# Kernel optimization log

Measured on AMD Instinct MI355X. Metric: run time of the kernel, lower is better.

The kernel has to match this reference:

```python
import jax, jax.numpy as jnp
import numpy as np

B, LT, D, H, DI = 8, 128, 512, 8, 2048
NMEM, LMEM = 1024, 64
DH = D // H
EPS = 1e-5
NEG = -1e9

def _ln(x, g, b):
    mu = x.mean(-1, keepdims=True)
    var = ((x - mu) ** 2).mean(-1, keepdims=True)
    return (x - mu) * jax.lax.rsqrt(var + EPS) * g + b

def _ffn(x, W1, b1, W2, b2):
    # PositionwiseFF with residual=True (dropout=0 / eval)
    return x + jax.nn.relu(x @ W1 + b1) @ W2 + b2

def setup_inputs():
    key = jax.random.key(0)
    ks = jax.random.split(key, 16)
    w = lambda i, shape: jax.random.normal(ks[i], shape, jnp.float32) * 0.02
    return {
        "dec_output": jax.random.normal(ks[0], (B, LT, D), jnp.float32),
        "mem_attn_out": jax.random.normal(ks[1], (B, LT, NMEM + 1), jnp.float32),
        "enc_out_mem": jax.random.normal(ks[2], (NMEM, LMEM, D), jnp.float32),
        "tgt_emb_mem": jax.random.normal(ks[3], (NMEM, LMEM, D), jnp.float32),
        "tgt_mask_mem": jax.random.randint(ks[4], (NMEM, LMEM), 0, 2, jnp.int32),
        "tgt_mask": jax.random.randint(ks[5], (B, LT), 0, 2, jnp.int32),
        "g0": jnp.ones((D,), jnp.float32), "be0": jnp.zeros((D,), jnp.float32),
        "g1": jnp.ones((D,), jnp.float32), "be1": jnp.zeros((D,), jnp.float32),
        "Wq": w(6, (D, D)), "bq": jnp.zeros((D,), jnp.float32),
        "Wk": w(7, (D, D)), "bk": jnp.zeros((D,), jnp.float32),
        "Wv": w(8, (D, D)), "bv": jnp.zeros((D,), jnp.float32),
        "Wo": w(9, (D, D)), "bo": jnp.zeros((D,), jnp.float32),
        "f1W1": w(10, (D, DI)), "f1b1": jnp.zeros((DI,), jnp.float32),
        "f1W2": w(11, (DI, D)), "f1b2": jnp.zeros((D,), jnp.float32),
        "f2W1": w(12, (D, DI)), "f2b1": jnp.zeros((DI,), jnp.float32),
        "f2W2": w(13, (DI, D)), "f2b2": jnp.zeros((D,), jnp.float32),
    }

def reference(dec_output, mem_attn_out, enc_out_mem, tgt_emb_mem, tgt_mask_mem, tgt_mask,
              g0, be0, g1, be1, Wq, bq, Wk, bk, Wv, bv, Wo, bo,
              f1W1, f1b1, f1W2, f1b2, f2W1, f2b1, f2W2, f2b2):
    x = _ln(dec_output, g0, be0)                       # [B,LT,D]
    N = B * LT
    samples = jnp.argmax(mem_attn_out, -1).reshape(N) - 1   # [-1, NMEM-1]
    valid = samples >= 0                               # [N]
    s = jnp.maximum(samples, 0)                        # clamp; masked later
    q = x.reshape(N, 1, D)
    # gather memory per selected query (torch compacts via unique; same math)
    k_in = enc_out_mem[s]                              # [N,LMEM,D]
    v_in = tgt_emb_mem[s]                              # [N,LMEM,D]
    kmask = tgt_mask_mem[s] != 0                       # True = valid key
    # multi-head attention, residual=True
    qh = (q @ Wq + bq).reshape(N, 1, H, DH).transpose(0, 2, 1, 3)     # [N,H,1,DH]
    kh = (k_in @ Wk + bk).reshape(N, LMEM, H, DH).transpose(0, 2, 1, 3)
    vh = (v_in @ Wv + bv).reshape(N, LMEM, H, DH).transpose(0, 2, 1, 3)
    scores = jnp.einsum('nhqd,nhkd->nhqk', qh, kh) / (DH ** 0.5)      # [N,H,1,LMEM]
    scores = jnp.where(kmask[:, None, None, :], scores, NEG)
    attn = jax.nn.softmax(scores, axis=-1)
    ctx = jnp.einsum('nhqk,nhkd->nhqd', attn, vh).transpose(0, 2, 1, 3).reshape(N, 1, D)
    st = q + ctx @ Wo + bo
    st = _ffn(st, f1W1, f1b1, f1W2, f1b2)
    st = _ln(st, g1, be1)
    # scatter back: positions with sample == -1 get zeros
    st = jnp.where(valid[:, None, None], st, 0.0)
    dec = x + st.reshape(B, LT, D)
    dec = _ffn(dec, f2W1, f2b1, f2W2, f2b2)
    return dec
```

## Files before the change

### kernel.cpp

```cpp
#include <hip/hip_runtime.h>
#include <math.h>

#define NQ   1024
#define DIM  512
#define NH   8
#define DHD  64
#define DFF  2048
#define LM   64

typedef __bf16 bf16x8 __attribute__((ext_vector_type(8)));
typedef float  f32x4  __attribute__((ext_vector_type(4)));

__device__ __forceinline__ unsigned short f2bf(float f) {
    unsigned u = __builtin_bit_cast(unsigned, f);
    return (unsigned short)((u + 0x7fffu + ((u >> 16) & 1u)) >> 16);
}
__device__ __forceinline__ float bflo(unsigned p) {
    return __builtin_bit_cast(float, p << 16);
}
__device__ __forceinline__ float bfhi(unsigned p) {
    return __builtin_bit_cast(float, p & 0xffff0000u);
}

__device__ __forceinline__ void gload16(const void* g, void* l) {
    __builtin_amdgcn_global_load_lds(
        (const __attribute__((address_space(1))) unsigned*)g,
        (__attribute__((address_space(3))) unsigned*)l, 16, 0, 0);
}

__device__ __forceinline__ float blk_sum(float v, volatile float* red) {
#pragma unroll
    for (int o = 32; o; o >>= 1) v += __shfl_down(v, o);
    __syncthreads();
    if ((threadIdx.x & 63) == 0) red[threadIdx.x >> 6] = v;
    __syncthreads();
    return red[0] + red[1] + red[2] + red[3];
}

struct PrepPtrs {
    const float* src[8];
    unsigned short* dst[8];
};
__global__ __launch_bounds__(256) void prep_ln0_k(
    PrepPtrs p,
    const float* __restrict__ dec_out, const float* __restrict__ attn_out,
    const float* __restrict__ g, const float* __restrict__ be,
    float* __restrict__ x, unsigned* __restrict__ xb, int* __restrict__ samples)
{
    __shared__ float tile[32][33];
    __shared__ float red[4];
    __shared__ float rv[4]; __shared__ int ri[4];
    const int bid = blockIdx.x;

    if (bid < 5120) {
        int m, lt;
        if (bid < 1024) { m = bid >> 8; lt = bid & 255; }
        else { m = 4 + ((bid - 1024) >> 10); lt = (bid - 1024) & 1023; }
        const int RS = (m < 4) ? 512 : ((m == 5 || m == 7) ? 2048 : 512);
        const int CS = (m < 4) ? 512 : ((m == 5 || m == 7) ? 512 : 2048);
        const int TC = CS >> 5;
        const int tr = lt / TC, tc = lt % TC;
        const float* s = p.src[m];
        unsigned short* d = p.dst[m];
        const int tx = threadIdx.x & 31, ty = threadIdx.x >> 5;
        if (m == 1) {
#pragma unroll
            for (int i = 0; i < 32; i += 8) {
                size_t idx = (size_t)(tr * 32 + ty + i) * CS + tc * 32 + tx;
                d[idx] = f2bf(s[idx]);
            }
        } else {
#pragma unroll
            for (int i = 0; i < 32; i += 8)
                tile[ty + i][tx] = s[(size_t)(tr * 32 + ty + i) * CS + tc * 32 + tx];
            __syncthreads();
#pragma unroll
            for (int i = 0; i < 32; i += 8)
                d[(size_t)(tc * 32 + ty + i) * RS + tr * 32 + tx] = f2bf(tile[tx][ty + i]);
        }
        return;
    }

    const int n = bid - 5120, t = threadIdx.x;
    float2 v = ((const float2*)(dec_out + (size_t)n * DIM))[t];
    float mu  = blk_sum(v.x + v.y, red) * (1.f / DIM);
    float dx = v.x - mu, dy = v.y - mu;
    float var = blk_sum(dx * dx + dy * dy, red) * (1.f / DIM);
    float rs = rsqrtf(var + 1e-5f);
    float2 gg = ((const float2*)g)[t], bb = ((const float2*)be)[t];
    float ox = dx * rs * gg.x + bb.x, oy = dy * rs * gg.y + bb.y;
    ((float2*)(x + (size_t)n * DIM))[t] = make_float2(ox, oy);
    xb[(size_t)n * 256 + t] = (unsigned)f2bf(ox) | ((unsigned)f2bf(oy) << 16);

    const float* ar = attn_out + (size_t)n * 1025;
    float bv = -INFINITY; int bi = 0x7fffffff;
    for (int i = t; i < 1025; i += 256) {
        float val = ar[i];
        if (val > bv || (val == bv && i < bi)) { bv = val; bi = i; }
    }
#pragma unroll
    for (int o = 32; o; o >>= 1) {
        float ov = __shfl_down(bv, o); int oi = __shfl_down(bi, o);
        if (ov > bv || (ov == bv && oi < bi)) { bv = ov; bi = oi; }
    }
    if ((t & 63) == 0) { rv[t >> 6] = bv; ri[t >> 6] = bi; }
    __syncthreads();
    if (t == 0) {
#pragma unroll
        for (int w = 1; w < 4; ++w)
            if (rv[w] > bv || (rv[w] == bv && ri[w] < bi)) { bv = rv[w]; bi = ri[w]; }
        samples[n] = bi - 1;
    }
}

template<bool RELU, bool BIAS, bool RES, bool WF32, bool WBF>
__global__ __launch_bounds__(256) void mfma_gemm(
    const unsigned short* __restrict__ A, const unsigned short* __restrict__ Bt,
    float* __restrict__ Cf, unsigned short* __restrict__ Cb,
    const float* __restrict__ bias, const float* __restrict__ res,
    int K, int lda, int ldb, int ldc,
    int sA, int sB, int sC, int sBias)
{
    __shared__ unsigned short Ab[2][64 * 64];
    __shared__ unsigned short Bb[2][64 * 64];
    const int t = threadIdx.x, lane = t & 63, wid = t >> 6;
    const int nx = gridDim.x;
    const int fid = blockIdx.y * nx + blockIdx.x;
    const int cpx = (nx * gridDim.y) >> 3;
    const int f2 = (fid & 7) * cpx + (fid >> 3);
    const int bn = (f2 % nx) * 64, bm = (f2 / nx) * 64, bz = blockIdx.z;
    const unsigned short* Abase = A + (size_t)bz * sA + (size_t)bm * lda;
    const unsigned short* Bbase = Bt + (size_t)bz * sB + (size_t)bn * ldb;

    const int r0 = wid * 16 + (lane >> 3);
    const int cbs = lane & 7;

#define STAGE_T(buf, base, ld, kt)                                              \
    {                                                                           \
        int r_ = r0;                                                            \
        gload16(base + (size_t)r_ * ld + (kt) * 64 + ((cbs ^ (r_ & 7)) << 3),   \
                &buf[(wid * 2 + 0) * 512]);                                     \
        r_ = r0 + 8;                                                            \
        gload16(base + (size_t)r_ * ld + (kt) * 64 + ((cbs ^ (r_ & 7)) << 3),   \
                &buf[(wid * 2 + 1) * 512]);                                     \
    }

    const int lr = lane & 15, lg = lane >> 4;
    const int wr = (wid >> 1) * 32, wc = (wid & 1) * 32;
    const int mA0 = wr + lr, mA1 = wr + 16 + lr;
    const int nB0 = wc + lr, nB1 = wc + 16 + lr;
    f32x4 acc[2][2] = {};

#define COMPUTE(b)                                                              \
    _Pragma("unroll")                                                           \
    for (int kk = 0; kk < 2; ++kk) {                                            \
        const int kb = kk * 4 + lg;                                             \
        bf16x8 a0 = *(const bf16x8*)&Ab[b][mA0 * 64 + ((kb ^ (mA0 & 7)) << 3)]; \
        bf16x8 a1 = *(const bf16x8*)&Ab[b][mA1 * 64 + ((kb ^ (mA1 & 7)) << 3)]; \
        bf16x8 b0 = *(const bf16x8*)&Bb[b][nB0 * 64 + ((kb ^ (nB0 & 7)) << 3)]; \
        bf16x8 b1 = *(const bf16x8*)&Bb[b][nB1 * 64 + ((kb ^ (nB1 & 7)) << 3)]; \
        acc[0][0] = __builtin_amdgcn_mfma_f32_16x16x32_bf16(a0, b0, acc[0][0], 0, 0, 0); \
        acc[0][1] = __builtin_amdgcn_mfma_f32_16x16x32_bf16(a0, b1, acc[0][1], 0, 0, 0); \
        acc[1][0] = __builtin_amdgcn_mfma_f32_16x16x32_bf16(a1, b0, acc[1][0], 0, 0, 0); \
        acc[1][1] = __builtin_amdgcn_mfma_f32_16x16x32_bf16(a1, b1, acc[1][1], 0, 0, 0); \
    }

    STAGE_T(Ab[0], Abase, lda, 0);
    STAGE_T(Bb[0], Bbase, ldb, 0);
    __syncthreads();
    const int NT = K >> 6;
    int cur = 0;
    for (int kt = 0; kt < NT; ++kt) {
        if (kt + 1 < NT) {
            STAGE_T(Ab[cur ^ 1], Abase, lda, kt + 1);
            STAGE_T(Bb[cur ^ 1], Bbase, ldb, kt + 1);
        }
        if (cur == 0) { COMPUTE(0); } else { COMPUTE(1); }
        __syncthreads();
        cur ^= 1;
    }

#pragma unroll
    for (int fm = 0; fm < 2; ++fm)
#pragma unroll
    for (int fn = 0; fn < 2; ++fn) {
        const int col = bn + wc + fn * 16 + lr;
        float bia = BIAS ? bias[bz * sBias + col] : 0.f;
#pragma unroll
        for (int r = 0; r < 4; ++r) {
            const int row = bm + wr + fm * 16 + lg * 4 + r;
            const size_t ci = (size_t)bz * sC + (size_t)row * ldc + col;
            float v = acc[fm][fn][r] + bia;
            if (RES) v += res[(size_t)row * ldc + col];
            if (RELU) v = fmaxf(v, 0.f);
            if (WF32) Cf[ci] = v;
            if (WBF)  Cb[ci] = f2bf(v);
        }
    }
#undef STAGE_T
#undef COMPUTE
}

__global__ __launch_bounds__(512) void attn_fused_k(
    const unsigned short* __restrict__ u_bf, const float* __restrict__ enc,
    const float* __restrict__ vemb, const int* __restrict__ maskmem,
    const int* __restrict__ samples, unsigned* __restrict__ a_bf)
{
    __shared__ float S_lds[8 * 68];
    __shared__ uint4 P_lds[64];
    __shared__ int Msk_lds[64];
    const int n = blockIdx.x, t = threadIdx.x;
    const int lane = t & 63, w = t >> 6;
    int s = samples[n]; if (s < 0) s = 0;

    float2 pfv[8];
    const float2* vb = (const float2*)(vemb + (size_t)s * (LM * DIM)) + (t - 256);

    if (w >= 4) {
#pragma unroll
        for (int i = 0; i < 8; ++i) pfv[i] = vb[(size_t)i * 256];
        if (w == 4) Msk_lds[lane] = maskmem[(size_t)s * LM + lane];
    } else {
        const float4* kb = (const float4*)(enc + (size_t)s * (LM * DIM));
        const int key = w * 16 + (lane & 15);
        const int lg = lane >> 4;
        const int h = lane & 15;
        const int base = key * 128 + lg * 2;
        float4 pf[4][2];
#pragma unroll
        for (int ss = 0; ss < 4; ++ss) {
            pf[ss][0] = kb[base + ss * 8];
            pf[ss][1] = kb[base + ss * 8 + 1];
        }
        const unsigned short* ub = u_bf + (size_t)n * 4096 + (size_t)(h & 7) * 512;
        f32x4 acc = {};
#pragma unroll
        for (int step = 0; step < 16; ++step) {
            float4 a0 = pf[step & 3][0], a1 = pf[step & 3][1];
            if (step + 4 < 16) {
                pf[step & 3][0] = kb[base + (step + 4) * 8];
                pf[step & 3][1] = kb[base + (step + 4) * 8 + 1];
            }
            bf16x8 af;
            af[0] = (__bf16)a0.x; af[1] = (__bf16)a0.y;
            af[2] = (__bf16)a0.z; af[3] = (__bf16)a0.w;
            af[4] = (__bf16)a1.x; af[5] = (__bf16)a1.y;
            af[6] = (__bf16)a1.z; af[7] = (__bf16)a1.w;
            bf16x8 bfr = *(const bf16x8*)&ub[(step * 4 + lg) * 8];
            acc = __builtin_amdgcn_mfma_f32_16x16x32_bf16(af, bfr, acc, 0, 0, 0);
        }
        if (h < 8) {
#pragma unroll
            for (int r = 0; r < 4; ++r)
                S_lds[h * 68 + w * 16 + lg * 4 + r] = acc[r];
        }
    }
    __syncthreads();

    if (w < 4) {
#pragma unroll
        for (int hh = 0; hh < 2; ++hh) {
            const int h2 = w + hh * 4;
            float sc = S_lds[h2 * 68 + lane] * 0.125f;
            sc = (Msk_lds[lane] != 0) ? sc : -1e9f;
            float m = sc;
#pragma unroll
            for (int o = 32; o; o >>= 1) m = fmaxf(m, __shfl_xor(m, o));
            float e = __expf(sc - m);
            float su = e;
#pragma unroll
            for (int o = 32; o; o >>= 1) su += __shfl_xor(su, o);
            ((unsigned short*)P_lds)[lane * 8 + h2] = f2bf(e / su);
        }
    }
    __syncthreads();

    if (w >= 4) {
        float2 acc8[8];
#pragma unroll
        for (int hh = 0; hh < 8; ++hh) acc8[hh] = make_float2(0.f, 0.f);
#pragma unroll 8
        for (int k = 0; k < 64; ++k) {
            float2 v = pfv[k & 7];
            if (k + 8 < 64) pfv[k & 7] = vb[(size_t)(k + 8) * 256];
            uint4 pr = P_lds[k];
            float p0 = bflo(pr.x), p1 = bfhi(pr.x);
            float p2 = bflo(pr.y), p3 = bfhi(pr.y);
            float p4 = bflo(pr.z), p5 = bfhi(pr.z);
            float p6 = bflo(pr.w), p7 = bfhi(pr.w);
            acc8[0].x = fmaf(p0, v.x, acc8[0].x); acc8[0].y = fmaf(p0, v.y, acc8[0].y);
            acc8[1].x = fmaf(p1, v.x, acc8[1].x); acc8[1].y = fmaf(p1, v.y, acc8[1].y);
            acc8[2].x = fmaf(p2, v.x, acc8[2].x); acc8[2].y = fmaf(p2, v.y, acc8[2].y);
            acc8[3].x = fmaf(p3, v.x, acc8[3].x); acc8[3].y = fmaf(p3, v.y, acc8[3].y);
            acc8[4].x = fmaf(p4, v.x, acc8[4].x); acc8[4].y = fmaf(p4, v.y, acc8[4].y);
            acc8[5].x = fmaf(p5, v.x, acc8[5].x); acc8[5].y = fmaf(p5, v.y, acc8[5].y);
            acc8[6].x = fmaf(p6, v.x, acc8[6].x); acc8[6].y = fmaf(p6, v.y, acc8[6].y);
            acc8[7].x = fmaf(p7, v.x, acc8[7].x); acc8[7].y = fmaf(p7, v.y, acc8[7].y);
        }
        unsigned* an = a_bf + (size_t)n * 2048 + (t - 256);
#pragma unroll
        for (int hh = 0; hh < 8; ++hh)
            an[hh * 256] = (unsigned)f2bf(acc8[hh].x) | ((unsigned)f2bf(acc8[hh].y) << 16);
    }
}

__global__ __launch_bounds__(256) void ln1_mask_add_k(
    const float* __restrict__ t1p, const float* __restrict__ st0,
    const float* __restrict__ b2, const float* __restrict__ g,
    const float* __restrict__ be, const int* __restrict__ samples,
    const float* __restrict__ x, float* __restrict__ dec, unsigned* __restrict__ decb)
{
    __shared__ float red[4];
    const int n = blockIdx.x, t = threadIdx.x;
    const size_t off = (size_t)n * DIM + t * 2;
    float2 p0 = *(const float2*)&t1p[off];
    float2 p1 = *(const float2*)&t1p[(size_t)NQ * DIM + off];
    float2 s0 = *(const float2*)&st0[off];
    float2 b2v = ((const float2*)b2)[t];
    float2 v = make_float2(p0.x + p1.x + s0.x + b2v.x, p0.y + p1.y + s0.y + b2v.y);
    float mu  = blk_sum(v.x + v.y, red) * (1.f / DIM);
    float dx = v.x - mu, dy = v.y - mu;
    float var = blk_sum(dx * dx + dy * dy, red) * (1.f / DIM);
    float rs = rsqrtf(var + 1e-5f);
    float2 gg = ((const float2*)g)[t], bb = ((const float2*)be)[t];
    float sx = dx * rs * gg.x + bb.x, sy = dy * rs * gg.y + bb.y;
    if (samples[n] < 0) { sx = 0.f; sy = 0.f; }
    float2 xx = *(const float2*)&x[off];
    float ox = xx.x + sx, oy = xx.y + sy;
    *(float2*)&dec[off] = make_float2(ox, oy);
    decb[(size_t)n * 256 + t] = (unsigned)f2bf(ox) | ((unsigned)f2bf(oy) << 16);
}

extern "C" void kernel_launch(void* const* d_in, const int* in_sizes, int n_in,
                              void* d_out, int out_size, void* d_ws, size_t ws_size,
                              hipStream_t stream)
{
    const float* dec_output = (const float*)d_in[0];
    const float* mem_attn   = (const float*)d_in[1];
    const float* enc_mem    = (const float*)d_in[2];
    const float* temb_mem   = (const float*)d_in[3];
    const int*   mask_mem   = (const int*)d_in[4];
    const float* g0  = (const float*)d_in[6];
    const float* be0 = (const float*)d_in[7];
    const float* g1  = (const float*)d_in[8];
    const float* be1 = (const float*)d_in[9];
    const float* Wq  = (const float*)d_in[10];
    const float* bq  = (const float*)d_in[11];
    const float* Wk  = (const float*)d_in[12];
    const float* Wv  = (const float*)d_in[14];
    const float* bv  = (const float*)d_in[15];
    const float* Wo  = (const float*)d_in[16];
    const float* bo  = (const float*)d_in[17];
    const float* f1W1 = (const float*)d_in[18];
    const float* f1b1 = (const float*)d_in[19];
    const float* f1W2 = (const float*)d_in[20];
    const float* f1b2 = (const float*)d_in[21];
    const float* f2W1 = (const float*)d_in[22];
    const float* f2b1 = (const float*)d_in[23];
    const float* f2W2 = (const float*)d_in[24];
    const float* f2b2 = (const float*)d_in[25];
    float* out = (float*)d_out;

    float* ws = (float*)d_ws;
    float*          x_f   = ws + 0;
    unsigned*       x_b   = (unsigned*)(ws + 524288);
    unsigned short* qh_b  = (unsigned short*)(ws + 786432);
    unsigned short* u_b   = (unsigned short*)(ws + 1048576);
    unsigned short* a_b   = (unsigned short*)(ws + 3145728);
    unsigned short* wqt   = (unsigned short*)(ws + 7340032);
    unsigned short* wkc   = (unsigned short*)(ws + 7471104);
    unsigned short* wvt   = (unsigned short*)(ws + 7602176);
    unsigned short* wot   = (unsigned short*)(ws + 7733248);
    unsigned short* f1w1t = (unsigned short*)(ws + 7864320);
    unsigned short* f1w2t = (unsigned short*)(ws + 8388608);
    unsigned short* f2w1t = (unsigned short*)(ws + 8912896);
    unsigned short* f2w2t = (unsigned short*)(ws + 9437184);
    int*            smp   = (int*)(ws + 9961472);
    float*          t1p_f = ws + 9962496;
    float*          st0_f = (float*)u_b + 0;
    unsigned short* st0_b = (unsigned short*)((float*)u_b + 524288);
    float*          dec_f = (float*)u_b + 655360;
    unsigned*       dec_b = (unsigned*)((float*)u_b + 1179648);
    unsigned short* h1_b  = a_b;
    unsigned short* h2_b  = (unsigned short*)((float*)a_b + 1048576);

    PrepPtrs pp;
    pp.src[0] = Wq;   pp.dst[0] = wqt;
    pp.src[1] = Wk;   pp.dst[1] = wkc;
    pp.src[2] = Wv;   pp.dst[2] = wvt;
    pp.src[3] = Wo;   pp.dst[3] = wot;
    pp.src[4] = f1W1; pp.dst[4] = f1w1t;
    pp.src[5] = f1W2; pp.dst[5] = f1w2t;
    pp.src[6] = f2W1; pp.dst[6] = f2w1t;
    pp.src[7] = f2W2; pp.dst[7] = f2w2t;
    prep_ln0_k<<<5120 + NQ, 256, 0, stream>>>(pp, dec_output, mem_attn, g0, be0,
                                              x_f, x_b, smp);
    mfma_gemm<false, true, false, false, true><<<dim3(8, 16, 1), 256, 0, stream>>>(
        (const unsigned short*)x_b, wqt, nullptr, qh_b, bq, nullptr,
        DIM, DIM, DIM, DIM, 0, 0, 0, 0);
    mfma_gemm<false, false, false, false, true><<<dim3(8, 16, NH), 256, 0, stream>>>(
        qh_b, wkc, nullptr, u_b, nullptr, nullptr,
        DHD, DIM, DIM, NH * DIM, DHD, DHD, DIM, 0);
    attn_fused_k<<<NQ, 512, 0, stream>>>(u_b, enc_mem, temb_mem, mask_mem, smp,
                                         (unsigned*)a_b);
    mfma_gemm<false, true, false, false, true><<<dim3(1, 16, NH), 256, 0, stream>>>(
        a_b, wvt, nullptr, qh_b, bv, nullptr,
        DIM, NH * DIM, DIM, DIM, DIM, DHD * DIM, DHD, DHD);
    mfma_gemm<false, true, true, true, true><<<dim3(8, 16, 1), 256, 0, stream>>>(
        qh_b, wot, st0_f, st0_b, bo, x_f, DIM, DIM, DIM, DIM, 0, 0, 0, 0);
    mfma_gemm<true, true, false, false, true><<<dim3(32, 16, 1), 256, 0, stream>>>(
        st0_b, f1w1t, nullptr, h1_b, f1b1, nullptr, DIM, DIM, DIM, DFF, 0, 0, 0, 0);
    mfma_gemm<false, false, false, true, false><<<dim3(8, 16, 2), 256, 0, stream>>>(
        h1_b, f1w2t, t1p_f, nullptr, nullptr, nullptr,
        1024, DFF, DFF, DIM, 1024, 1024, NQ * DIM, 0);
    ln1_mask_add_k<<<NQ, 256, 0, stream>>>(t1p_f, st0_f, f1b2, g1, be1, smp,
                                           x_f, dec_f, dec_b);
    mfma_gemm<true, true, false, false, true><<<dim3(32, 16, 1), 256, 0, stream>>>(
        (const unsigned short*)dec_b, f2w1t, nullptr, h2_b, f2b1, nullptr,
        DIM, DIM, DIM, DFF, 0, 0, 0, 0);
    mfma_gemm<false, true, true, true, false><<<dim3(8, 16, 1), 256, 0, stream>>>(
        h2_b, f2w2t, out, nullptr, f2b2, dec_f, DFF, DFF, DFF, DIM, 0, 0, 0, 0);

    (void)in_sizes; (void)n_in; (void)out_size; (void)ws_size;
}
```

Before: 149.9 us.

## Group queries by memory slot and process query pairs sharing one gathered memory

Adds a single-block kernel that buckets the 1024 queries by their sampled memory index and builds a list of query pairs sharing the same slot. The attention kernel then handles two queries per block, loading the 64x512 key and value rows once and using the idle half of the 16-column MFMA tile for the second query. This targets the redundant global reads of enc/temb memory, which dominate the attention stage. It adds an extra serial launch, and because argmax hits over 1024 slots are sparse, few queries share a slot, so most pairs may be singletons and the saving could be small.

```diff
diff --git a/kernel.cpp b/kernel.cpp
--- a/kernel.cpp
+++ b/kernel.cpp
@@ -7,6 +7,7 @@
 #define DHD  64
 #define DFF  2048
 #define LM   64
+#define NMEM 1024
 
 typedef __bf16 bf16x8 __attribute__((ext_vector_type(8)));
 typedef float  f32x4  __attribute__((ext_vector_type(4)));
@@ -110,6 +111,78 @@
         for (int w = 1; w < 4; ++w)
             if (rv[w] > bv || (rv[w] == bv && ri[w] < bi)) { bv = rv[w]; bi = ri[w]; }
         samples[n] = bi - 1;
+    }
+}
+
+__global__ __launch_bounds__(1024) void group_build_k(
+    const int* __restrict__ samples, int2* __restrict__ plist,
+    int* __restrict__ npairs)
+{
+    __shared__ int cnt[NMEM];
+    __shared__ int base[NMEM];
+    __shared__ int qls[NQ];
+    __shared__ int wsum[16];
+    __shared__ int wsum2[16];
+    const int t = threadIdx.x;
+    const int lane = t & 63, w = t >> 6;
+    cnt[t] = 0;
+    __syncthreads();
+    int s = samples[t]; if (s < 0) s = 0;
+    atomicAdd(&cnt[s], 1);
+    __syncthreads();
+    const int c = cnt[t];
+    int v = c;
+#pragma unroll
+    for (int o = 1; o < 64; o <<= 1) {
+        int u = __shfl_up(v, o);
+        if (lane >= o) v += u;
+    }
+    if (lane == 63) wsum[w] = v;
+    __syncthreads();
+    if (w == 0) {
+        int x = (lane < 16) ? wsum[lane] : 0;
+#pragma unroll
+        for (int o = 1; o < 16; o <<= 1) {
+            int u = __shfl_up(x, o);
+            if (lane >= o) x += u;
+        }
+        if (lane < 16) wsum[lane] = x;
+    }
+    __syncthreads();
+    const int start = v - c + (w ? wsum[w - 1] : 0);
+    base[t] = start;
+    __syncthreads();
+    cnt[t] = 0;
+    __syncthreads();
+    int pos = atomicAdd(&cnt[s], 1);
+    qls[base[s] + pos] = t;
+    const int pc = (c + 1) >> 1;
+    int pv = pc;
+#pragma unroll
+    for (int o = 1; o < 64; o <<= 1) {
+        int u = __shfl_up(pv, o);
+        if (lane >= o) pv += u;
+    }
+    if (lane == 63) wsum2[w] = pv;
+    __syncthreads();
+    if (w == 0) {
+        int x = (lane < 16) ? wsum2[lane] : 0;
+#pragma unroll
+        for (int o = 1; o < 16; o <<= 1) {
+            int u = __shfl_up(x, o);
+            if (lane >= o) x += u;
+        }
+        if (lane < 16) wsum2[lane] = x;
+    }
+    __syncthreads();
+    const int pstart = pv - pc + (w ? wsum2[w - 1] : 0);
+    if (t == NMEM - 1) *npairs = pstart + pc;
+    __syncthreads();
+    const int b = base[t];
+    for (int j = 0; j < pc; ++j) {
+        int qa = qls[b + 2 * j];
+        int qb = (2 * j + 1 < c) ? qls[b + 2 * j + 1] : qa;
+        plist[pstart + j] = make_int2(qa, qb);
     }
 }
 
@@ -204,14 +277,18 @@
 __global__ __launch_bounds__(512) void attn_fused_k(
     const unsigned short* __restrict__ u_bf, const float* __restrict__ enc,
     const float* __restrict__ vemb, const int* __restrict__ maskmem,
-    const int* __restrict__ samples, unsigned* __restrict__ a_bf)
+    const int* __restrict__ samples, const int2* __restrict__ plist,
+    const int* __restrict__ npairs, unsigned* __restrict__ a_bf)
 {
-    __shared__ float S_lds[8 * 68];
-    __shared__ uint4 P_lds[64];
+    __shared__ float S_lds[16 * 68];
+    __shared__ uint4 P_lds[2][64];
     __shared__ int Msk_lds[64];
-    const int n = blockIdx.x, t = threadIdx.x;
-    const int lane = t & 63, w = t >> 6;
-    int s = samples[n]; if (s < 0) s = 0;
+    const int pid = blockIdx.x;
+    if (pid >= *npairs) return;
+    const int2 pq = plist[pid];
+    const int qa = pq.x, qb = pq.y;
+    int s = samples[qa]; if (s < 0) s = 0;
+    const int t = threadIdx.x, lane = t & 63, w = t >> 6;
 
     float2 pfv[8];
     const float2* vb = (const float2*)(vemb + (size_t)s * (LM * DIM)) + (t - 256);
@@ -232,7 +309,8 @@
             pf[ss][0] = kb[base + ss * 8];
             pf[ss][1] = kb[base + ss * 8 + 1];
         }
-        const unsigned short* ub = u_bf + (size_t)n * 4096 + (size_t)(h & 7) * 512;
+        const int qsel = (h < 8) ? qa : qb;
+        const unsigned short* ub = u_bf + (size_t)qsel * 4096 + (size_t)(h & 7) * 512;
         f32x4 acc = {};
 #pragma unroll
         for (int step = 0; step < 16; ++step) {
@@ -249,19 +327,18 @@
             bf16x8 bfr = *(const bf16x8*)&ub[(step * 4 + lg) * 8];
             acc = __builtin_amdgcn_mfma_f32_16x16x32_bf16(af, bfr, acc, 0, 0, 0);
         }
-        if (h < 8) {
-#pragma unroll
-            for (int r = 0; r < 4; ++r)
-                S_lds[h * 68 + w * 16 + lg * 4 + r] = acc[r];
-        }
+#pragma unroll
+        for (int r = 0; r < 4; ++r)
+            S_lds[h * 68 + w * 16 + lg * 4 + r] = acc[r];
     }
     __syncthreads();
 
     if (w < 4) {
 #pragma unroll
-        for (int hh = 0; hh < 2; ++hh) {
-            const int h2 = w + hh * 4;
-            float sc = S_lds[h2 * 68 + lane] * 0.125f;
+        for (int i = 0; i < 4; ++i) {
+            const int slot = w + i * 4;
+            const int qq = slot >> 3, h2 = slot & 7;
+            float sc = S_lds[slot * 68 + lane] * 0.125f;
             sc = (Msk_lds[lane] != 0) ? sc : -1e9f;
             float m = sc;
 #pragma unroll
@@ -270,37 +347,55 @@
             float su = e;
 #pragma unroll
             for (int o = 32; o; o >>= 1) su += __shfl_xor(su, o);
-            ((unsigned short*)P_lds)[lane * 8 + h2] = f2bf(e / su);
+            ((unsigned short*)P_lds)[(qq * 64 + lane) * 8 + h2] = f2bf(e / su);
         }
     }
     __syncthreads();
 
     if (w >= 4) {
-        float2 acc8[8];
-#pragma unroll
-        for (int hh = 0; hh < 8; ++hh) acc8[hh] = make_float2(0.f, 0.f);
-#pragma unroll 8
+        float2 accA[8], accB[8];
+#pragma unroll
+        for (int hh = 0; hh < 8; ++hh) {
+            accA[hh] = make_float2(0.f, 0.f);
+            accB[hh] = make_float2(0.f, 0.f);
+        }
+#pragma unroll 4
         for (int k = 0; k < 64; ++k) {
             float2 v = pfv[k & 7];
             if (k + 8 < 64) pfv[k & 7] = vb[(size_t)(k + 8) * 256];
-            uint4 pr = P_lds[k];
-            float p0 = bflo(pr.x), p1 = bfhi(pr.x);
-            float p2 = bflo(pr.y), p3 = bfhi(pr.y);
-            float p4 = bflo(pr.z), p5 = bfhi(pr.z);
-            float p6 = bflo(pr.w), p7 = bfhi(pr.w);
-            acc8[0].x = fmaf(p0, v.x, acc8[0].x); acc8[0].y = fmaf(p0, v.y, acc8[0].y);
-            acc8[1].x = fmaf(p1, v.x, acc8[1].x); acc8[1].y = fmaf(p1, v.y, acc8[1].y);
-            acc8[2].x = fmaf(p2, v.x, acc8[2].x); acc8[2].y = fmaf(p2, v.y, acc8[2].y);
-            acc8[3].x = fmaf(p3, v.x, acc8[3].x); acc8[3].y = fmaf(p3, v.y, acc8[3].y);
-            acc8[4].x = fmaf(p4, v.x, acc8[4].x); acc8[4].y = fmaf(p4, v.y, acc8[4].y);
-            acc8[5].x = fmaf(p5, v.x, acc8[5].x); acc8[5].y = fmaf(p5, v.y, acc8[5].y);
-            acc8[6].x = fmaf(p6, v.x, acc8[6].x); acc8[6].y = fmaf(p6, v.y, acc8[6].y);
-            acc8[7].x = fmaf(p7, v.x, acc8[7].x); acc8[7].y = fmaf(p7, v.y, acc8[7].y);
-        }
-        unsigned* an = a_bf + (size_t)n * 2048 + (t - 256);
+            uint4 pa = P_lds[0][k];
+            uint4 pb = P_lds[1][k];
+            float a0 = bflo(pa.x), a1 = bfhi(pa.x), a2 = bflo(pa.y), a3 = bfhi(pa.y);
+            float a4 = bflo(pa.z), a5 = bfhi(pa.z), a6 = bflo(pa.w), a7 = bfhi(pa.w);
+            float b0 = bflo(pb.x), b1 = bfhi(pb.x), b2 = bflo(pb.y), b3 = bfhi(pb.y);
+            float b4 = bflo(pb.z), b5 = bfhi(pb.z), b6 = bflo(pb.w), b7 = bfhi(pb.w);
+            accA[0].x = fmaf(a0, v.x, accA[0].x); accA[0].y = fmaf(a0, v.y, accA[0].y);
+            accA[1].x = fmaf(a1, v.x, accA[1].x); accA[1].y = fmaf(a1, v.y, accA[1].y);
+            accA[2].x = fmaf(a2, v.x, accA[2].x); accA[2].y = fmaf(a2, v.y, accA[2].y);
+            accA[3].x = fmaf(a3, v.x, accA[3].x); accA[3].y = fmaf(a3, v.y, accA[3].y);
+            accA[4].x = fmaf(a4, v.x, accA[4].x); accA[4].y = fmaf(a4, v.y, accA[4].y);
+            accA[5].x = fmaf(a5, v.x, accA[5].x); accA[5].y = fmaf(a5, v.y, accA[5].y);
+            accA[6].x = fmaf(a6, v.x, accA[6].x); accA[6].y = fmaf(a6, v.y, accA[6].y);
+            accA[7].x = fmaf(a7, v.x, accA[7].x); accA[7].y = fmaf(a7, v.y, accA[7].y);
+            accB[0].x = fmaf(b0, v.x, accB[0].x); accB[0].y = fmaf(b0, v.y, accB[0].y);
+            accB[1].x = fmaf(b1, v.x, accB[1].x); accB[1].y = fmaf(b1, v.y, accB[1].y);
+            accB[2].x = fmaf(b2, v.x, accB[2].x); accB[2].y = fmaf(b2, v.y, accB[2].y);
+            accB[3].x = fmaf(b3, v.x, accB[3].x); accB[3].y = fmaf(b3, v.y, accB[3].y);
+            accB[4].x = fmaf(b4, v.x, accB[4].x); accB[4].y = fmaf(b4, v.y, accB[4].y);
+            accB[5].x = fmaf(b5, v.x, accB[5].x); accB[5].y = fmaf(b5, v.y, accB[5].y);
+            accB[6].x = fmaf(b6, v.x, accB[6].x); accB[6].y = fmaf(b6, v.y, accB[6].y);
+            accB[7].x = fmaf(b7, v.x, accB[7].x); accB[7].y = fmaf(b7, v.y, accB[7].y);
+        }
+        unsigned* an = a_bf + (size_t)qa * 2048 + (t - 256);
 #pragma unroll
         for (int hh = 0; hh < 8; ++hh)
-            an[hh * 256] = (unsigned)f2bf(acc8[hh].x) | ((unsigned)f2bf(acc8[hh].y) << 16);
+            an[hh * 256] = (unsigned)f2bf(accA[hh].x) | ((unsigned)f2bf(accA[hh].y) << 16);
+        if (qb != qa) {
+            unsigned* bn2 = a_bf + (size_t)qb * 2048 + (t - 256);
+#pragma unroll
+            for (int hh = 0; hh < 8; ++hh)
+                bn2[hh * 256] = (unsigned)f2bf(accB[hh].x) | ((unsigned)f2bf(accB[hh].y) << 16);
+        }
     }
 }
 
@@ -377,6 +472,8 @@
     unsigned short* f2w2t = (unsigned short*)(ws + 9437184);
     int*            smp   = (int*)(ws + 9961472);
     float*          t1p_f = ws + 9962496;
+    int2*           plist = (int2*)(ws + 11011072);
+    int*            npair = (int*)(ws + 11013120);
     float*          st0_f = (float*)u_b + 0;
     unsigned short* st0_b = (unsigned short*)((float*)u_b + 524288);
     float*          dec_f = (float*)u_b + 655360;
@@ -395,6 +492,7 @@
     pp.src[7] = f2W2; pp.dst[7] = f2w2t;
     prep_ln0_k<<<5120 + NQ, 256, 0, stream>>>(pp, dec_output, mem_attn, g0, be0,
                                               x_f, x_b, smp);
+    group_build_k<<<1, 1024, 0, stream>>>(smp, plist, npair);
     mfma_gemm<false, true, false, false, true><<<dim3(8, 16, 1), 256, 0, stream>>>(
         (const unsigned short*)x_b, wqt, nullptr, qh_b, bq, nullptr,
         DIM, DIM, DIM, DIM, 0, 0, 0, 0);
@@ -402,7 +500,7 @@
         qh_b, wkc, nullptr, u_b, nullptr, nullptr,
         DHD, DIM, DIM, NH * DIM, DHD, DHD, DIM, 0);
     attn_fused_k<<<NQ, 512, 0, stream>>>(u_b, enc_mem, temb_mem, mask_mem, smp,
-                                         (unsigned*)a_b);
+                                         plist, npair, (unsigned*)a_b);
     mfma_gemm<false, true, false, false, true><<<dim3(1, 16, NH), 256, 0, stream>>>(
         a_b, wvt, nullptr, qh_b, bv, nullptr,
         DIM, NH * DIM, DIM, DIM, DIM, DHD * DIM, DHD, DHD);
```

Result: slower. 177.3 us (+18.3%).
